# Kernel tuning notes

Hardware: AMD Instinct MI355X
Metric: run time of the kernel (lower is better)

Reference implementation:

```python
import jax, jax.numpy as jnp
import numpy as np

NEG_BIG = -9e15  # matches torch's -9000000000000000.0 masked-fill value
ALPHA = 0.2      # LeakyReLU negative slope


def setup_inputs() -> dict:
    key = jax.random.key(0)
    k1, k2, k3, k4 = jax.random.split(key, 4)
    N, F_in, F_out = 8192, 128, 64
    h = jax.random.normal(k1, (N, F_in), dtype=jnp.float32)
    adj = jax.random.randint(k2, (N, N), 0, 2).astype(jnp.float32)
    # Glorot(gain=1.414)-scale params
    W = jax.random.normal(k3, (F_in, F_out), dtype=jnp.float32) * (1.414 * np.sqrt(2.0 / (F_in + F_out)))
    a = jax.random.normal(k4, (2 * F_out, 1), dtype=jnp.float32) * (1.414 * np.sqrt(2.0 / (2 * F_out + 1)))
    return {"h": h, "adj": adj, "W": W, "a": a}


def reference(h, adj, W, a):
    F_out = W.shape[1]
    Wh = h @ W                               # [N, F_out]
    Wh1 = Wh @ a[:F_out, :]                  # [N, 1]
    Wh2 = Wh @ a[F_out:, :]                  # [N, 1]
    e = jax.nn.leaky_relu(Wh1 + Wh2.T, negative_slope=ALPHA)  # [N, N]
    attention = jnp.where(adj > 0, e, NEG_BIG)
    attention = jax.nn.softmax(attention, axis=1)
    # dropout omitted (eval mode / p applied only in training)
    h_prime = attention @ Wh                 # [N, F_out]
    return jax.nn.elu(h_prime)               # concat=True -> ELU
```

## Files before the change

### kernel.cpp

```cpp
#include <hip/hip_runtime.h>
#include <hip/hip_bf16.h>

#define N 8192
#define FIN 128
#define FOUT 64
#define ALPHA 0.2f
#define LOG2E 1.44269504f
#define JSPLIT 4
#define JSPAN (N / JSPLIT)
#define STJ 256
#define NST (JSPAN / STJ)

typedef __attribute__((ext_vector_type(8))) short short8;
typedef __attribute__((ext_vector_type(4))) float f32x4;

static __device__ __forceinline__ unsigned fkey(float x) {
    unsigned u = __float_as_uint(x);
    return (u >> 31) ? ~u : (u | 0x80000000u);
}
static __device__ __forceinline__ float fdecode(unsigned k) {
    unsigned u = (k & 0x80000000u) ? (k & 0x7FFFFFFFu) : ~k;
    return __uint_as_float(u);
}
static __device__ __forceinline__ void gll16(const float* g, float* l) {
    __builtin_amdgcn_global_load_lds(
        (const __attribute__((address_space(1))) unsigned int*)g,
        (__attribute__((address_space(3))) unsigned int*)l, 16, 0, 0);
}

__global__ __launch_bounds__(256) void k_prep(const float* __restrict__ h,
                                              const float* __restrict__ W,
                                              const float* __restrict__ a,
                                              float* __restrict__ Wh,
                                              float* __restrict__ s2,
                                              float* __restrict__ t2,
                                              unsigned* __restrict__ keys) {
    __shared__ float lH[16 * FIN];
    __shared__ float lW[FIN * FOUT];
    __shared__ float red[8];
    const int tid = threadIdx.x;
    const int r0 = blockIdx.x * 16;
    {
        const float4* src = (const float4*)(h + (size_t)r0 * FIN);
        float4* dst = (float4*)lH;
        for (int i = tid; i < 16 * FIN / 4; i += 256) dst[i] = src[i];
        const float4* ws_ = (const float4*)W;
        float4* dw = (float4*)lW;
        for (int i = tid; i < FIN * FOUT / 4; i += 256) dw[i] = ws_[i];
    }
    __syncthreads();
    const int wave = tid >> 6, lane = tid & 63;
    float acc[4] = {0.f, 0.f, 0.f, 0.f};
    for (int k = 0; k < FIN; ++k) {
        float wv = lW[k * FOUT + lane];
#pragma unroll
        for (int r = 0; r < 4; ++r)
            acc[r] = fmaf(lH[(wave * 4 + r) * FIN + k], wv, acc[r]);
    }
    const float a1 = a[lane], a2 = a[FOUT + lane];
    float smx = -1e30f, tmx = -1e30f;
#pragma unroll
    for (int r = 0; r < 4; ++r) {
        int row = r0 + wave * 4 + r;
        Wh[(size_t)row * FOUT + lane] = acc[r];
        float sv = acc[r] * a1, tv = acc[r] * a2;
#pragma unroll
        for (int off = 32; off; off >>= 1) {
            sv += __shfl_xor(sv, off);
            tv += __shfl_xor(tv, off);
        }
        sv *= LOG2E; tv *= LOG2E;
        if (lane == 0) { s2[row] = sv; t2[row] = tv; }
        smx = fmaxf(smx, sv);
        tmx = fmaxf(tmx, tv);
    }
    if (lane == 0) { red[wave] = smx; red[4 + wave] = tmx; }
    __syncthreads();
    if (tid == 0) {
        float ms = fmaxf(fmaxf(red[0], red[1]), fmaxf(red[2], red[3]));
        float mt = fmaxf(fmaxf(red[4], red[5]), fmaxf(red[6], red[7]));
        atomicMax(keys + 0, fkey(ms));
        atomicMax(keys + 1, fkey(mt));
    }
}

__global__ __launch_bounds__(256) void k_pack(const float* __restrict__ Wh,
                                              __hip_bfloat16* __restrict__ WhB) {
    const int c = blockIdx.x;
    const int tn = threadIdx.x >> 6;
    const int lane = threadIdx.x & 63;
    const int quad = lane >> 4, l16 = lane & 15;
    const float* src = Wh + ((size_t)(c * 32 + quad * 8)) * FOUT + tn * 16 + l16;
    union { unsigned short u[8]; short8 v; } frag;
#pragma unroll
    for (int e = 0; e < 8; ++e) {
        __hip_bfloat16 b = __float2bfloat16(src[(size_t)e * FOUT]);
        frag.u[e] = *(unsigned short*)&b;
    }
    *(short8*)&WhB[(((size_t)c * 4 + tn) * 64 + lane) * 8] = frag.v;
}

__global__ __launch_bounds__(256) void k_attn(const float* __restrict__ adj,
                                              const __hip_bfloat16* __restrict__ WhB,
                                              const float* __restrict__ s2,
                                              const float* __restrict__ t2,
                                              const unsigned* __restrict__ keys,
                                              float* __restrict__ acc_ws,
                                              float* __restrict__ l_ws) {
    __shared__ float bufA[2][8 * 512];
    __shared__ float tl[JSPAN];
    const int wave = threadIdx.x >> 6, lane = threadIdx.x & 63;
    const int quad = lane >> 4, l16 = lane & 15;
    const int i0 = blockIdx.x * 16;
    const int jb = blockIdx.y * JSPAN;
    const int u0 = 2 * wave;

    {
        const float4* src = (const float4*)(t2 + jb);
        float4* dst = (float4*)tl;
        for (int i = threadIdx.x; i < JSPAN / 4; i += 256) dst[i] = src[i];
    }
    const float* gaw = adj + (size_t)(i0 + l16) * N + jb + quad * 8;
    gll16(gaw + u0 * 32,      &bufA[0][u0 * 512]);
    gll16(gaw + u0 * 32 + 4,  &bufA[0][u0 * 512 + 256]);
    gll16(gaw + u0 * 32 + 32, &bufA[0][(u0 + 1) * 512]);
    gll16(gaw + u0 * 32 + 36, &bufA[0][(u0 + 1) * 512 + 256]);

    const float mraw = fdecode(keys[0]) + fdecode(keys[1]);
    const float mm = mraw > 0.f ? mraw : ALPHA * mraw;
    const float sm = s2[i0 + l16];
    const short8* BF = (const short8*)WhB;

    f32x4 acc0 = {0,0,0,0}, acc1 = {0,0,0,0}, acc2 = {0,0,0,0}, acc3 = {0,0,0,0};
    float lsum = 0.f;
    __syncthreads();

    for (int st = 0; st < NST; ++st) {
        const int b = st & 1;
        const size_t kc = (size_t)(blockIdx.y * (JSPAN / 32) + st * 8 + u0) * 4;
        short8 B00 = BF[(kc + 0) * 64 + lane];
        short8 B01 = BF[(kc + 1) * 64 + lane];
        short8 B02 = BF[(kc + 2) * 64 + lane];
        short8 B03 = BF[(kc + 3) * 64 + lane];
        short8 B10 = BF[(kc + 4) * 64 + lane];
        short8 B11 = BF[(kc + 5) * 64 + lane];
        short8 B12 = BF[(kc + 6) * 64 + lane];
        short8 B13 = BF[(kc + 7) * 64 + lane];
        __builtin_amdgcn_sched_barrier(0);
        if (st + 1 < NST) {
            const float* g = gaw + (st + 1) * STJ + u0 * 32;
            float* d = &bufA[b ^ 1][u0 * 512];
            gll16(g, d);
            gll16(g + 4, d + 256);
            gll16(g + 32, d + 512);
            gll16(g + 36, d + 768);
        }
        __builtin_amdgcn_sched_barrier(0);
#pragma unroll
        for (int uu = 0; uu < 2; ++uu) {
            const int ul = u0 + uu;
            const float* Au = &bufA[b][ul * 512];
            float4 alo = *(const float4*)(Au + lane * 4);
            float4 ahi = *(const float4*)(Au + 256 + lane * 4);
            const float* Tp = tl + st * STJ + ul * 32 + quad * 8;
            float4 tlo = *(const float4*)Tp;
            float4 thi = *(const float4*)(Tp + 4);
            union { __hip_bfloat162 h2[4]; short8 v; } af;
#pragma unroll
            for (int pp = 0; pp < 4; ++pp) {
                float a0 = (pp < 2) ? ((const float*)&alo)[2 * pp]     : ((const float*)&ahi)[2 * pp - 4];
                float a1 = (pp < 2) ? ((const float*)&alo)[2 * pp + 1] : ((const float*)&ahi)[2 * pp - 3];
                float t0 = (pp < 2) ? ((const float*)&tlo)[2 * pp]     : ((const float*)&thi)[2 * pp - 4];
                float t1 = (pp < 2) ? ((const float*)&tlo)[2 * pp + 1] : ((const float*)&thi)[2 * pp - 3];
                float x0 = sm + t0,                x1 = sm + t1;
                float le0 = fmaxf(x0, ALPHA * x0), le1 = fmaxf(x1, ALPHA * x1);
                float p0 = a0 * exp2f(le0 - mm),   p1 = a1 * exp2f(le1 - mm);
                __hip_bfloat162 pb = __float22bfloat162_rn(make_float2(p0, p1));
                af.h2[pp] = pb;
                lsum += __bfloat162float(pb.x) + __bfloat162float(pb.y);
            }
            if (uu == 0) {
                acc0 = __builtin_amdgcn_mfma_f32_16x16x32_bf16(af.v, B00, acc0, 0, 0, 0);
                acc1 = __builtin_amdgcn_mfma_f32_16x16x32_bf16(af.v, B01, acc1, 0, 0, 0);
                acc2 = __builtin_amdgcn_mfma_f32_16x16x32_bf16(af.v, B02, acc2, 0, 0, 0);
                acc3 = __builtin_amdgcn_mfma_f32_16x16x32_bf16(af.v, B03, acc3, 0, 0, 0);
            } else {
                acc0 = __builtin_amdgcn_mfma_f32_16x16x32_bf16(af.v, B10, acc0, 0, 0, 0);
                acc1 = __builtin_amdgcn_mfma_f32_16x16x32_bf16(af.v, B11, acc1, 0, 0, 0);
                acc2 = __builtin_amdgcn_mfma_f32_16x16x32_bf16(af.v, B12, acc2, 0, 0, 0);
                acc3 = __builtin_amdgcn_mfma_f32_16x16x32_bf16(af.v, B13, acc3, 0, 0, 0);
            }
        }
        __syncthreads();
    }

    lsum += __shfl_xor(lsum, 16);
    lsum += __shfl_xor(lsum, 32);

    float* accr = &bufA[0][0];
    float* shlp = tl;
    *(f32x4*)&accr[((wave * 4 + 0) * 64 + lane) * 4] = acc0;
    *(f32x4*)&accr[((wave * 4 + 1) * 64 + lane) * 4] = acc1;
    *(f32x4*)&accr[((wave * 4 + 2) * 64 + lane) * 4] = acc2;
    *(f32x4*)&accr[((wave * 4 + 3) * 64 + lane) * 4] = acc3;
    if (lane < 16) shlp[wave * 16 + lane] = lsum;
    __syncthreads();

    const int tile = wave;
    f32x4 tot = {0, 0, 0, 0};
#pragma unroll
    for (int w = 0; w < 4; ++w) {
        f32x4 c = *(const f32x4*)&accr[((w * 4 + tile) * 64 + lane) * 4];
        tot[0] += c[0]; tot[1] += c[1]; tot[2] += c[2]; tot[3] += c[3];
    }
#pragma unroll
    for (int r = 0; r < 4; ++r) {
        int row = quad * 4 + r;
        atomicAdd(&acc_ws[(size_t)(i0 + row) * FOUT + tile * 16 + l16], tot[r]);
    }
    if (wave == 0 && lane < 16) {
        float lv = shlp[lane] + shlp[16 + lane] + shlp[32 + lane] + shlp[48 + lane];
        atomicAdd(&l_ws[i0 + lane], lv);
    }
}

__global__ __launch_bounds__(256) void k_final(const float* __restrict__ acc_ws,
                                               const float* __restrict__ l_ws,
                                               float* __restrict__ out) {
    const int idx = blockIdx.x * 256 + threadIdx.x;
    const int row = idx >> 4;
    const float inv = 1.0f / l_ws[row];
    float4 a = ((const float4*)acc_ws)[idx];
    float4 o;
#pragma unroll
    for (int r = 0; r < 4; ++r) {
        float v = ((const float*)&a)[r] * inv;
        ((float*)&o)[r] = v > 0.f ? v : (exp2f(v * LOG2E) - 1.f);
    }
    ((float4*)out)[idx] = o;
}

extern "C" void kernel_launch(void* const* d_in, const int* in_sizes, int n_in,
                              void* d_out, int out_size, void* d_ws, size_t ws_size,
                              hipStream_t stream) {
    const float* h   = (const float*)d_in[0];
    const float* adj = (const float*)d_in[1];
    const float* W   = (const float*)d_in[2];
    const float* a   = (const float*)d_in[3];
    float* out = (float*)d_out;

    char* base = (char*)d_ws;
    float* Wh = (float*)base;                        base += (size_t)N * FOUT * 4;
    __hip_bfloat16* WhB = (__hip_bfloat16*)base;     base += (size_t)N * FOUT * 2;
    float* s2 = (float*)base;                        base += (size_t)N * 4;
    float* t2 = (float*)base;                        base += (size_t)N * 4 + 1024;
    float* acc_ws = (float*)base;                    base += (size_t)N * FOUT * 4;
    float* l_ws = (float*)base;                      base += (size_t)N * 4;
    unsigned* keys = (unsigned*)base;

    hipMemsetAsync(acc_ws, 0, ((size_t)N * FOUT + N) * 4 + 2 * sizeof(unsigned), stream);
    k_prep<<<N / 16, 256, 0, stream>>>(h, W, a, Wh, s2, t2, keys);
    k_pack<<<N / 32, 256, 0, stream>>>(Wh, WhB);
    dim3 ag(N / 16, JSPLIT);
    k_attn<<<ag, 256, 0, stream>>>(adj, WhB, s2, t2, keys, acc_ws, l_ws);
    k_final<<<N * FOUT / 4 / 256, 256, 0, stream>>>(acc_ws, l_ws, out);
}
```

Baseline: 398.1 us.

## Drop column split, fuse normalization and ELU into attention kernel, remove per-stage barrier

The attention kernel now covers the full column range per row tile instead of splitting it four ways. The final normalization and ELU are written straight to the output. This removes the atomic accumulation into workspace, the large workspace memset and the separate finalize kernel. The per-stage __syncthreads is replaced with explicit vmcnt waits, since each wave only reads the LDS slices it loaded itself. In exchange the grid shrinks from 2048 to 512 blocks and LDS per block grows (full t2 row of 32KB). That lowers occupancy and latency hiding for the bandwidth-heavy adj stream.

Measured after the change: 403.3 us. No clear change (+1.3%).

```diff
diff --git a/kernel.cpp b/kernel.cpp
--- a/kernel.cpp
+++ b/kernel.cpp
@@ -6,8 +6,7 @@
 #define FOUT 64
 #define ALPHA 0.2f
 #define LOG2E 1.44269504f
-#define JSPLIT 4
-#define JSPAN (N / JSPLIT)
+#define JSPAN N
 #define STJ 256
 #define NST (JSPAN / STJ)
 
@@ -105,27 +104,26 @@
                                               const float* __restrict__ s2,
                                               const float* __restrict__ t2,
                                               const unsigned* __restrict__ keys,
-                                              float* __restrict__ acc_ws,
-                                              float* __restrict__ l_ws) {
+                                              float* __restrict__ out) {
     __shared__ float bufA[2][8 * 512];
     __shared__ float tl[JSPAN];
+    __shared__ float sred[64];
     const int wave = threadIdx.x >> 6, lane = threadIdx.x & 63;
     const int quad = lane >> 4, l16 = lane & 15;
     const int i0 = blockIdx.x * 16;
-    const int jb = blockIdx.y * JSPAN;
     const int u0 = 2 * wave;
 
-    {
-        const float4* src = (const float4*)(t2 + jb);
-        float4* dst = (float4*)tl;
-        for (int i = threadIdx.x; i < JSPAN / 4; i += 256) dst[i] = src[i];
-    }
-    const float* gaw = adj + (size_t)(i0 + l16) * N + jb + quad * 8;
+    const float* gaw = adj + (size_t)(i0 + l16) * N + quad * 8;
     gll16(gaw + u0 * 32,      &bufA[0][u0 * 512]);
     gll16(gaw + u0 * 32 + 4,  &bufA[0][u0 * 512 + 256]);
     gll16(gaw + u0 * 32 + 32, &bufA[0][(u0 + 1) * 512]);
     gll16(gaw + u0 * 32 + 36, &bufA[0][(u0 + 1) * 512 + 256]);
 
+    {
+        const float4* src = (const float4*)t2;
+        float4* dst = (float4*)tl;
+        for (int i = threadIdx.x; i < JSPAN / 4; i += 256) dst[i] = src[i];
+    }
     const float mraw = fdecode(keys[0]) + fdecode(keys[1]);
     const float mm = mraw > 0.f ? mraw : ALPHA * mraw;
     const float sm = s2[i0 + l16];
@@ -137,7 +135,7 @@
 
     for (int st = 0; st < NST; ++st) {
         const int b = st & 1;
-        const size_t kc = (size_t)(blockIdx.y * (JSPAN / 32) + st * 8 + u0) * 4;
+        const size_t kc = (size_t)(st * 8 + u0) * 4;
         short8 B00 = BF[(kc + 0) * 64 + lane];
         short8 B01 = BF[(kc + 1) * 64 + lane];
         short8 B02 = BF[(kc + 2) * 64 + lane];
@@ -154,6 +152,10 @@
             gll16(g + 4, d + 256);
             gll16(g + 32, d + 512);
             gll16(g + 36, d + 768);
+            __builtin_amdgcn_sched_barrier(0);
+            asm volatile("s_waitcnt vmcnt(12)" ::: "memory");
+        } else {
+            asm volatile("s_waitcnt vmcnt(8)" ::: "memory");
         }
         __builtin_amdgcn_sched_barrier(0);
 #pragma unroll
@@ -191,19 +193,17 @@
                 acc3 = __builtin_amdgcn_mfma_f32_16x16x32_bf16(af.v, B13, acc3, 0, 0, 0);
             }
         }
-        __syncthreads();
     }
 
     lsum += __shfl_xor(lsum, 16);
     lsum += __shfl_xor(lsum, 32);
 
     float* accr = &bufA[0][0];
-    float* shlp = tl;
     *(f32x4*)&accr[((wave * 4 + 0) * 64 + lane) * 4] = acc0;
     *(f32x4*)&accr[((wave * 4 + 1) * 64 + lane) * 4] = acc1;
     *(f32x4*)&accr[((wave * 4 + 2) * 64 + lane) * 4] = acc2;
     *(f32x4*)&accr[((wave * 4 + 3) * 64 + lane) * 4] = acc3;
-    if (lane < 16) shlp[wave * 16 + lane] = lsum;
+    if (lane < 16) sred[wave * 16 + lane] = lsum;
     __syncthreads();
 
     const int tile = wave;
@@ -216,28 +216,11 @@
 #pragma unroll
     for (int r = 0; r < 4; ++r) {
         int row = quad * 4 + r;
-        atomicAdd(&acc_ws[(size_t)(i0 + row) * FOUT + tile * 16 + l16], tot[r]);
-    }
-    if (wave == 0 && lane < 16) {
-        float lv = shlp[lane] + shlp[16 + lane] + shlp[32 + lane] + shlp[48 + lane];
-        atomicAdd(&l_ws[i0 + lane], lv);
-    }
-}
-
-__global__ __launch_bounds__(256) void k_final(const float* __restrict__ acc_ws,
-                                               const float* __restrict__ l_ws,
-                                               float* __restrict__ out) {
-    const int idx = blockIdx.x * 256 + threadIdx.x;
-    const int row = idx >> 4;
-    const float inv = 1.0f / l_ws[row];
-    float4 a = ((const float4*)acc_ws)[idx];
-    float4 o;
-#pragma unroll
-    for (int r = 0; r < 4; ++r) {
-        float v = ((const float*)&a)[r] * inv;
-        ((float*)&o)[r] = v > 0.f ? v : (exp2f(v * LOG2E) - 1.f);
-    }
-    ((float4*)out)[idx] = o;
+        float lv = sred[row] + sred[16 + row] + sred[32 + row] + sred[48 + row];
+        float v = tot[r] / lv;
+        out[(size_t)(i0 + row) * FOUT + tile * 16 + l16] =
+            v > 0.f ? v : (exp2f(v * LOG2E) - 1.f);
+    }
 }
 
 extern "C" void kernel_launch(void* const* d_in, const int* in_sizes, int n_in,
@@ -254,14 +237,10 @@
     __hip_bfloat16* WhB = (__hip_bfloat16*)base;     base += (size_t)N * FOUT * 2;
     float* s2 = (float*)base;                        base += (size_t)N * 4;
     float* t2 = (float*)base;                        base += (size_t)N * 4 + 1024;
-    float* acc_ws = (float*)base;                    base += (size_t)N * FOUT * 4;
-    float* l_ws = (float*)base;                      base += (size_t)N * 4;
     unsigned* keys = (unsigned*)base;
 
-    hipMemsetAsync(acc_ws, 0, ((size_t)N * FOUT + N) * 4 + 2 * sizeof(unsigned), stream);
+    hipMemsetAsync(keys, 0, 2 * sizeof(unsigned), stream);
     k_prep<<<N / 16, 256, 0, stream>>>(h, W, a, Wh, s2, t2, keys);
     k_pack<<<N / 32, 256, 0, stream>>>(Wh, WhB);
-    dim3 ag(N / 16, JSPLIT);
-    k_attn<<<ag, 256, 0, stream>>>(adj, WhB, s2, t2, keys, acc_ws, l_ws);
-    k_final<<<N * FOUT / 4 / 256, 256, 0, stream>>>(acc_ws, l_ws, out);
-}
+    k_attn<<<N / 16, 256, 0, stream>>>(adj, WhB, s2, t2, keys, out);
+}
```
